# Kernel optimization log

Measured on AMD Instinct MI355X. Metric: run time of the kernel, lower is better.

The kernel has to match this reference:

```python
import jax, jax.numpy as jnp
import numpy as np

D, H, W = 160, 192, 160


def _grid_sample_3d(vol, grid):
    """torch F.grid_sample (3D, bilinear/trilinear, padding='zeros', align_corners=False).
    vol: [B,C,D,H,W]; grid: [B,Do,Ho,Wo,3], last dim ordered (x,y,z) in [-1,1]."""
    B, C, Dv, Hv, Wv = vol.shape
    x, y, z = grid[..., 0], grid[..., 1], grid[..., 2]
    # align_corners=False unnormalization
    ix = ((x + 1.0) * Wv - 1.0) * 0.5
    iy = ((y + 1.0) * Hv - 1.0) * 0.5
    iz = ((z + 1.0) * Dv - 1.0) * 0.5
    fx, fy, fz = jnp.floor(ix), jnp.floor(iy), jnp.floor(iz)
    wx, wy, wz = ix - fx, iy - fy, iz - fz
    ix0, iy0, iz0 = fx.astype(jnp.int32), fy.astype(jnp.int32), fz.astype(jnp.int32)
    vol_flat = vol.reshape(B, C, Dv * Hv * Wv)
    out_sp = x.shape[1:]  # (Do, Ho, Wo)

    def gather(zi, yi, xi):
        inb = ((zi >= 0) & (zi < Dv) & (yi >= 0) & (yi < Hv) & (xi >= 0) & (xi < Wv))
        lin = ((jnp.clip(zi, 0, Dv - 1) * Hv + jnp.clip(yi, 0, Hv - 1)) * Wv
               + jnp.clip(xi, 0, Wv - 1)).reshape(B, -1)
        vals = jax.vmap(lambda v, i: v[:, i])(vol_flat, lin)  # [B,C,N]
        return vals.reshape((B, C) + out_sp) * inb[:, None].astype(vol.dtype)

    out = jnp.zeros((B, C) + tuple(out_sp), vol.dtype)
    # fixed 8-corner trilinear accumulation
    for dz, wz_ in ((0, 1.0 - wz), (1, wz)):
        for dy, wy_ in ((0, 1.0 - wy), (1, wy)):
            for dx, wx_ in ((0, 1.0 - wx), (1, wx)):
                w = (wz_ * wy_ * wx_)[:, None]  # [B,1,Do,Ho,Wo]
                out = out + w * gather(iz0 + dz, iy0 + dy, ix0 + dx)
    return out


def _voxel_grid():
    gd, gh, gw = jnp.meshgrid(jnp.arange(D, dtype=jnp.float32),
                              jnp.arange(H, dtype=jnp.float32),
                              jnp.arange(W, dtype=jnp.float32), indexing='ij')
    return jnp.stack([gd, gh, gw])[None]  # [1,3,D,H,W], channels (d,h,w)


def _to_xyz(t):
    # [B,3,D,H,W] channels (d,h,w) -> [B,D,H,W,3] channels (x,y,z)
    return jnp.moveaxis(t, 1, -1)[..., ::-1]


def setup_inputs() -> dict:
    key = jax.random.key(0)
    k1, k2, k3 = jax.random.split(key, 3)
    src = jax.random.normal(k1, (1, 1, D, H, W), dtype=jnp.float32)
    flow1 = jax.random.normal(k2, (1, 3, D, H, W), dtype=jnp.float32)
    flow2 = jax.random.normal(k3, (1, 3, D, H, W), dtype=jnp.float32)
    range_flow = jnp.float32(0.4)
    return {"src": src, "flow1": flow1, "flow2": flow2, "range_flow": range_flow}


def reference(src, flow1, flow2, range_flow):
    grid = _voxel_grid()  # voxel-coordinate identity grid
    # NOTE: grid2 is intentionally NOT normalized to [-1,1] (faithful to source quirk)
    grid2 = _to_xyz(grid + flow2 * range_flow)
    flow1_warped = _grid_sample_3d(flow1, grid2)
    out_flow = flow1_warped + flow2
    denom = jnp.array([D - 1, H - 1, W - 1], jnp.float32).reshape(1, 3, 1, 1, 1)
    new_locs_total = 2.0 * ((grid + out_flow * range_flow) / denom - 0.5)
    deform_2_img = _grid_sample_3d(src, _to_xyz(new_locs_total))
    return deform_2_img, out_flow
```

## Files before the change

kernel.cpp:

```cpp
#include <hip/hip_runtime.h>

constexpr int Dv = 160, Hv = 192, Wv = 160;
constexpr int NN = Dv * Hv * Wv;

constexpr int TW = 32, TH = 8, TD = 8;
constexpr int SX = TW + 5, SY = TH + 5, SZ = TD + 5;
constexpr int SLEN = SX * SY * SZ;
constexpr int SITER = (SLEN + 255) / 256;
constexpr int SPAD = SITER * 256;

__device__ __forceinline__ void tri3_rare(const float* __restrict__ v,
                                          float gx, float gy, float gz,
                                          float& o0, float& o1, float& o2) {
  o0 = 0.0f; o1 = 0.0f; o2 = 0.0f;
  float ix = ((gx + 1.0f) * (float)Wv - 1.0f) * 0.5f;
  float iy = ((gy + 1.0f) * (float)Hv - 1.0f) * 0.5f;
  float iz = ((gz + 1.0f) * (float)Dv - 1.0f) * 0.5f;
  float fx = floorf(ix), fy = floorf(iy), fz = floorf(iz);
  int x0 = (int)fx, y0 = (int)fy, z0 = (int)fz;
  if (x0 < -1 || x0 >= Wv || y0 < -1 || y0 >= Hv || z0 < -1 || z0 >= Dv)
    return;
  float wx = ix - fx, wy = iy - fy, wz = iz - fz;
#pragma unroll
  for (int c = 0; c < 8; ++c) {
    const int dz = (c >> 2) & 1, dy = (c >> 1) & 1, dx = c & 1;
    int zi = z0 + dz, yi = y0 + dy, xi = x0 + dx;
    if ((unsigned)zi < (unsigned)Dv && (unsigned)yi < (unsigned)Hv &&
        (unsigned)xi < (unsigned)Wv) {
      float wgt = (dz ? wz : 1.0f - wz) * (dy ? wy : 1.0f - wy) *
                  (dx ? wx : 1.0f - wx);
      int lin = (zi * Hv + yi) * Wv + xi;
      o0 += wgt * v[lin];
      o1 += wgt * v[NN + lin];
      o2 += wgt * v[2 * NN + lin];
    }
  }
}

__global__ __launch_bounds__(256)
void st_tiled_kernel(const float* __restrict__ src,
                     const float* __restrict__ flow1,
                     const float* __restrict__ flow2,
                     const float* __restrict__ rfp,
                     float* __restrict__ out) {
  __shared__ float tile[SPAD];

  const int tid = threadIdx.x;
  const int bx0 = blockIdx.x * TW;
  const int by0 = blockIdx.y * TH;
  const int bz0 = blockIdx.z * TD;
  const float rf = rfp[0];

  const int lw = tid & (TW - 1);
  const int lh = tid >> 5;
  const int w = bx0 + lw;
  const int h = by0 + lh;

  float f2d[TD], f2h[TD], f2w[TD];
#pragma unroll
  for (int ld = 0; ld < TD; ++ld) {
    int idx = ((bz0 + ld) * Hv + h) * Wv + w;
    f2d[ld] = flow2[idx];
    f2h[ld] = flow2[NN + idx];
    f2w[ld] = flow2[2 * NN + idx];
  }

  const int bxo = bx0 - 2, byo = by0 - 2, bzo = bz0 - 2;
#pragma unroll
  for (int i = 0; i < SITER; ++i) {
    int t = tid + i * 256;
    int tt = (i == SITER - 1) ? min(t, SLEN - 1) : t;
    int tz = tt / (SY * SX);
    int r = tt - tz * (SY * SX);
    int ty = r / SX;
    int tx = r - ty * SX;
    int gx = min(max(bxo + tx, 0), Wv - 1);
    int gy = min(max(byo + ty, 0), Hv - 1);
    int gz = min(max(bzo + tz, 0), Dv - 1);
    int g = (gz * Hv + gy) * Wv + gx;
    __builtin_amdgcn_global_load_lds(
        (const __attribute__((address_space(1))) void*)(src + g),
        (__attribute__((address_space(3))) void*)(tile + t), 4, 0, 0);
  }
  __syncthreads();

  const float wf = (float)w, hf = (float)h;
  constexpr float KX = (float)Wv / (float)(Wv - 1);
  constexpr float KY = (float)Hv / (float)(Hv - 1);
  constexpr float KZ = (float)Dv / (float)(Dv - 1);

#pragma unroll
  for (int ld = 0; ld < TD; ++ld) {
    const int d = bz0 + ld;
    const float df = (float)d;
    const int idx = (d * Hv + h) * Wv + w;

    float a0, a1, a2;
    tri3_rare(flow1, wf + rf * f2w[ld], hf + rf * f2h[ld], df + rf * f2d[ld],
              a0, a1, a2);

    float of_d = a0 + f2d[ld];
    float of_h = a1 + f2h[ld];
    float of_w = a2 + f2w[ld];

    out[NN + idx] = of_d;
    out[2 * NN + idx] = of_h;
    out[3 * NN + idx] = of_w;

    float ix = (wf + rf * of_w) * KX - 0.5f;
    float iy = (hf + rf * of_h) * KY - 0.5f;
    float iz = (df + rf * of_d) * KZ - 0.5f;

    float fx = floorf(ix), fy = floorf(iy), fz = floorf(iz);
    float wx = ix - fx, wy = iy - fy, wz = iz - fz;
    int x0 = (int)fx, y0 = (int)fy, z0 = (int)fz;

    float wx0 = ((unsigned)x0 < (unsigned)Wv) ? (1.0f - wx) : 0.0f;
    float wx1 = ((unsigned)(x0 + 1) < (unsigned)Wv) ? wx : 0.0f;
    float wy0 = ((unsigned)y0 < (unsigned)Hv) ? (1.0f - wy) : 0.0f;
    float wy1 = ((unsigned)(y0 + 1) < (unsigned)Hv) ? wy : 0.0f;
    float wz0 = ((unsigned)z0 < (unsigned)Dv) ? (1.0f - wz) : 0.0f;
    float wz1 = ((unsigned)(z0 + 1) < (unsigned)Dv) ? wz : 0.0f;

    int tx = x0 - bxo, ty = y0 - byo, tz = z0 - bzo;
    bool fast = ((unsigned)tx <= (unsigned)(SX - 2)) &
                ((unsigned)ty <= (unsigned)(SY - 2)) &
                ((unsigned)tz <= (unsigned)(SZ - 2));

    float v000, v001, v010, v011, v100, v101, v110, v111;
    if (fast) {
      int base = (tz * SY + ty) * SX + tx;
      v000 = tile[base];
      v001 = tile[base + 1];
      v010 = tile[base + SX];
      v011 = tile[base + SX + 1];
      v100 = tile[base + SY * SX];
      v101 = tile[base + SY * SX + 1];
      v110 = tile[base + SY * SX + SX];
      v111 = tile[base + SY * SX + SX + 1];
    } else {
      int xa0 = min(max(x0, 0), Wv - 1), xa1 = min(max(x0 + 1, 0), Wv - 1);
      int ya0 = min(max(y0, 0), Hv - 1), ya1 = min(max(y0 + 1, 0), Hv - 1);
      int za0 = min(max(z0, 0), Dv - 1), za1 = min(max(z0 + 1, 0), Dv - 1);
      int r00 = (za0 * Hv + ya0) * Wv;
      int r01 = (za0 * Hv + ya1) * Wv;
      int r10 = (za1 * Hv + ya0) * Wv;
      int r11 = (za1 * Hv + ya1) * Wv;
      v000 = src[r00 + xa0]; v001 = src[r00 + xa1];
      v010 = src[r01 + xa0]; v011 = src[r01 + xa1];
      v100 = src[r10 + xa0]; v101 = src[r10 + xa1];
      v110 = src[r11 + xa0]; v111 = src[r11 + xa1];
    }

    float c00 = v000 * wx0 + v001 * wx1;
    float c01 = v010 * wx0 + v011 * wx1;
    float c10 = v100 * wx0 + v101 * wx1;
    float c11 = v110 * wx0 + v111 * wx1;
    float c0 = c00 * wy0 + c01 * wy1;
    float c1 = c10 * wy0 + c11 * wy1;
    out[idx] = c0 * wz0 + c1 * wz1;
  }
}

extern "C" void kernel_launch(void* const* d_in, const int* in_sizes, int n_in,
                              void* d_out, int out_size, void* d_ws, size_t ws_size,
                              hipStream_t stream) {
  const float* src   = (const float*)d_in[0];
  const float* flow1 = (const float*)d_in[1];
  const float* flow2 = (const float*)d_in[2];
  const float* rfp   = (const float*)d_in[3];
  float* out = (float*)d_out;

  dim3 grid(Wv / TW, Hv / TH, Dv / TD);
  hipLaunchKernelGGL(st_tiled_kernel, grid, dim3(256), 0, stream,
                     src, flow1, flow2, rfp, out);
}
```

Before: 185.3 us.

## Vectorize LDS halo staging and split trilinear corner reads between LDS and global

Widens the halo tile's x extent to 40 with a 4-aligned origin, so each global_load_lds moves 16 bytes instead of 4, cutting staging instructions roughly fourfold. The sampling path now always reads the upper z-plane's four corners directly from global memory and takes only the lower plane from the LDS tile. That relaxes the z fast-path bound and splits gather traffic across LDS and cache. The risk is that the extra global loads per voxel may cost more than the LDS bandwidth and conflicts they relieve.

```diff
diff --git a/kernel.cpp b/kernel.cpp
--- a/kernel.cpp
+++ b/kernel.cpp
@@ -4,10 +4,11 @@
 constexpr int NN = Dv * Hv * Wv;
 
 constexpr int TW = 32, TH = 8, TD = 8;
-constexpr int SX = TW + 5, SY = TH + 5, SZ = TD + 5;
+constexpr int SX = 40, SY = 13, SZ = 13;
 constexpr int SLEN = SX * SY * SZ;
-constexpr int SITER = (SLEN + 255) / 256;
-constexpr int SPAD = SITER * 256;
+constexpr int SVEC = SLEN / 4;
+constexpr int SITER = (SVEC + 255) / 256;
+constexpr int SPAD = SITER * 256 * 4;
 
 __device__ __forceinline__ void tri3_rare(const float* __restrict__ v,
                                           float gx, float gy, float gz,
@@ -65,22 +66,23 @@
     f2w[ld] = flow2[2 * NN + idx];
   }
 
-  const int bxo = bx0 - 2, byo = by0 - 2, bzo = bz0 - 2;
+  const int bxo = bx0 - 4, byo = by0 - 2, bzo = bz0 - 2;
 #pragma unroll
   for (int i = 0; i < SITER; ++i) {
     int t = tid + i * 256;
-    int tt = (i == SITER - 1) ? min(t, SLEN - 1) : t;
-    int tz = tt / (SY * SX);
-    int r = tt - tz * (SY * SX);
+    int tt = (i == SITER - 1) ? min(t, SVEC - 1) : t;
+    int e = tt * 4;
+    int tz = e / (SY * SX);
+    int r = e - tz * (SY * SX);
     int ty = r / SX;
     int tx = r - ty * SX;
-    int gx = min(max(bxo + tx, 0), Wv - 1);
+    int gx = min(max(bxo + tx, 0), Wv - 4);
     int gy = min(max(byo + ty, 0), Hv - 1);
     int gz = min(max(bzo + tz, 0), Dv - 1);
     int g = (gz * Hv + gy) * Wv + gx;
     __builtin_amdgcn_global_load_lds(
         (const __attribute__((address_space(1))) void*)(src + g),
-        (__attribute__((address_space(3))) void*)(tile + t), 4, 0, 0);
+        (__attribute__((address_space(3))) void*)(tile + e), 16, 0, 0);
   }
   __syncthreads();
 
@@ -122,34 +124,33 @@
     float wz0 = ((unsigned)z0 < (unsigned)Dv) ? (1.0f - wz) : 0.0f;
     float wz1 = ((unsigned)(z0 + 1) < (unsigned)Dv) ? wz : 0.0f;
 
-    int tx = x0 - bxo, ty = y0 - byo, tz = z0 - bzo;
-    bool fast = ((unsigned)tx <= (unsigned)(SX - 2)) &
-                ((unsigned)ty <= (unsigned)(SY - 2)) &
-                ((unsigned)tz <= (unsigned)(SZ - 2));
+    int xa0 = min(max(x0, 0), Wv - 1), xa1 = min(max(x0 + 1, 0), Wv - 1);
+    int ya0 = min(max(y0, 0), Hv - 1), ya1 = min(max(y0 + 1, 0), Hv - 1);
 
-    float v000, v001, v010, v011, v100, v101, v110, v111;
+    int za1 = min(max(z0 + 1, 0), Dv - 1);
+    int r10 = (za1 * Hv + ya0) * Wv;
+    int r11 = (za1 * Hv + ya1) * Wv;
+    float v100 = src[r10 + xa0], v101 = src[r10 + xa1];
+    float v110 = src[r11 + xa0], v111 = src[r11 + xa1];
+
+    int txi = x0 - bxo, tyi = y0 - byo, tzi = z0 - bzo;
+    bool fast = ((unsigned)txi <= (unsigned)(SX - 2)) &
+                ((unsigned)tyi <= (unsigned)(SY - 2)) &
+                ((unsigned)tzi <= (unsigned)(SZ - 1));
+
+    float v000, v001, v010, v011;
     if (fast) {
-      int base = (tz * SY + ty) * SX + tx;
+      int base = (tzi * SY + tyi) * SX + txi;
       v000 = tile[base];
       v001 = tile[base + 1];
       v010 = tile[base + SX];
       v011 = tile[base + SX + 1];
-      v100 = tile[base + SY * SX];
-      v101 = tile[base + SY * SX + 1];
-      v110 = tile[base + SY * SX + SX];
-      v111 = tile[base + SY * SX + SX + 1];
     } else {
-      int xa0 = min(max(x0, 0), Wv - 1), xa1 = min(max(x0 + 1, 0), Wv - 1);
-      int ya0 = min(max(y0, 0), Hv - 1), ya1 = min(max(y0 + 1, 0), Hv - 1);
-      int za0 = min(max(z0, 0), Dv - 1), za1 = min(max(z0 + 1, 0), Dv - 1);
+      int za0 = min(max(z0, 0), Dv - 1);
       int r00 = (za0 * Hv + ya0) * Wv;
       int r01 = (za0 * Hv + ya1) * Wv;
-      int r10 = (za1 * Hv + ya0) * Wv;
-      int r11 = (za1 * Hv + ya1) * Wv;
       v000 = src[r00 + xa0]; v001 = src[r00 + xa1];
       v010 = src[r01 + xa0]; v011 = src[r01 + xa1];
-      v100 = src[r10 + xa0]; v101 = src[r10 + xa1];
-      v110 = src[r11 + xa0]; v111 = src[r11 + xa1];
     }
 
     float c00 = v000 * wx0 + v001 * wx1;
```

Result: no change. 187.0 us (+0.9%).
